# Performance work log

Measured on AMD Instinct MI355X. Metric: run time of the kernel, lower is better.

The kernel has to match this reference:

```python
import jax, jax.numpy as jnp
import numpy as np


def setup_inputs() -> dict:
    key = jax.random.key(0)
    kq, kk, kw, ku, kv = jax.random.split(key, 5)
    B, L, S, H = 32, 2, 4096, 1024
    scale = 1.0 / np.sqrt(H).astype(np.float32)
    return {
        "query": jax.random.normal(kq, (B, L, H), dtype=jnp.float32),
        "keys": jax.random.normal(kk, (B, S, H), dtype=jnp.float32),
        "W": jax.random.normal(kw, (H, H), dtype=jnp.float32) * scale,
        "U": jax.random.normal(ku, (H, H), dtype=jnp.float32) * scale,
        "V": jax.random.normal(kv, (1, H), dtype=jnp.float32) * scale,
    }


def reference(query, keys, W, U, V):
    # query: [B, L, H]; keys: [B, S, H]; torch Linear computes x @ W^T
    q = query[:, -1, :][:, None, :]                      # [B, 1, H]
    wq = jnp.tanh(jnp.einsum('bqh,oh->bqo', q, W))       # [B, 1, H] (tanh only on W q, per source)
    uk = jnp.einsum('bsh,oh->bso', keys, U)              # [B, S, H]
    scores = jnp.einsum('bsh,oh->bso', wq + uk, V)       # [B, S, 1]
    scores = scores[..., 0][:, None, :]                  # [B, 1, S]
    weight = jax.nn.softmax(scores, axis=-1)             # [B, 1, S]
    context = jnp.einsum('bqs,bsh->bqh', weight, keys)   # [B, 1, H]
    return (context, weight)
```

## Files before the change

### kernel.cpp

```cpp
#include <hip/hip_runtime.h>
#include <math.h>

#define HDIM   1024
#define BATCH  32
#define SEQ    4096
#define NB     32
#define SCHUNK (SEQ / NB)
#define NWAVES 4
#define RPW    4
#define PSTR   1028

#define OFF_V 0
#define OFF_P HDIM

__global__ __launch_bounds__(256) void veff_kernel(const float* __restrict__ U,
                                                   const float* __restrict__ V,
                                                   float* __restrict__ ws) {
    const int h  = blockIdx.x * 256 + threadIdx.x;
    const int o0 = blockIdx.y * 64;
    float acc = 0.f;
#pragma unroll 8
    for (int o = o0; o < o0 + 64; ++o) {
        acc += V[o] * U[(long)o * HDIM + h];
    }
    atomicAdd(&ws[OFF_V + h], acc);
}

__global__ __launch_bounds__(256) void score_ctx_kernel(const float* __restrict__ keys,
                                                        float* __restrict__ ws,
                                                        float* __restrict__ out) {
    const int bi    = blockIdx.x;
    const int b     = bi / NB;
    const int chunk = bi % NB;
    const int tid   = threadIdx.x;
    const int w     = tid >> 6;
    const int lane  = tid & 63;

    const float4* v4 = (const float4*)(ws + OFF_V);
    float4 vr[4];
#pragma unroll
    for (int c = 0; c < 4; ++c) vr[c] = v4[c * 64 + lane];

    const float4* k4 = (const float4*)keys;
    const long rowbase = (long)(b * SEQ + chunk * SCHUNK) * (HDIM / 4);

    float4 oacc[4];
#pragma unroll
    for (int c = 0; c < 4; ++c) oacc[c] = make_float4(0.f, 0.f, 0.f, 0.f);
    float l = 0.f;

    float* scores = out + (long)BATCH * HDIM + (long)b * SEQ + chunk * SCHUNK;

    for (int it = 0; it < SCHUNK / (RPW * NWAVES); ++it) {
        const int r0 = it * (RPW * NWAVES) + w * RPW;

        float4 ka[RPW][4];
#pragma unroll
        for (int r = 0; r < RPW; ++r)
#pragma unroll
            for (int c = 0; c < 4; ++c)
                ka[r][c] = k4[rowbase + (long)(r0 + r) * 256 + c * 64 + lane];

        float p[RPW];
#pragma unroll
        for (int r = 0; r < RPW; ++r) {
            float acc = 0.f;
#pragma unroll
            for (int c = 0; c < 4; ++c)
                acc += ka[r][c].x * vr[c].x + ka[r][c].y * vr[c].y
                     + ka[r][c].z * vr[c].z + ka[r][c].w * vr[c].w;
            p[r] = acc;
        }
#pragma unroll
        for (int off = 32; off; off >>= 1) {
#pragma unroll
            for (int r = 0; r < RPW; ++r) p[r] += __shfl_xor(p[r], off, 64);
        }
        if (lane == 0) {
            *(float4*)(scores + r0) = make_float4(p[0], p[1], p[2], p[3]);
        }

        float e[RPW];
#pragma unroll
        for (int r = 0; r < RPW; ++r) e[r] = __expf(p[r]);
        l += e[0] + e[1] + e[2] + e[3];

#pragma unroll
        for (int c = 0; c < 4; ++c) {
            oacc[c].x += e[0]*ka[0][c].x + e[1]*ka[1][c].x + e[2]*ka[2][c].x + e[3]*ka[3][c].x;
            oacc[c].y += e[0]*ka[0][c].y + e[1]*ka[1][c].y + e[2]*ka[2][c].y + e[3]*ka[3][c].y;
            oacc[c].z += e[0]*ka[0][c].z + e[1]*ka[1][c].z + e[2]*ka[2][c].z + e[3]*ka[3][c].z;
            oacc[c].w += e[0]*ka[0][c].w + e[1]*ka[1][c].w + e[2]*ka[2][c].w + e[3]*ka[3][c].w;
        }
    }

    __shared__ float lds_o[NWAVES][HDIM];
    __shared__ float lds_l[NWAVES];

    float4* lo4 = (float4*)lds_o[w];
#pragma unroll
    for (int c = 0; c < 4; ++c) lo4[c * 64 + lane] = oacc[c];
    if (lane == 0) lds_l[w] = l;
    __syncthreads();

    float* part = ws + OFF_P + (long)bi * PSTR;
#pragma unroll
    for (int k = 0; k < HDIM / 256; ++k) {
        const int h = tid + k * 256;
        part[4 + h] = lds_o[0][h] + lds_o[1][h] + lds_o[2][h] + lds_o[3][h];
    }
    if (tid == 0) part[0] = lds_l[0] + lds_l[1] + lds_l[2] + lds_l[3];
}

__global__ __launch_bounds__(256) void combine_kernel(const float* __restrict__ ws,
                                                      float* __restrict__ out) {
    const int b   = blockIdx.x;
    const int tid = threadIdx.x;
    const float* part = ws + OFF_P + (long)b * NB * PSTR;

    float lg = 0.f;
#pragma unroll
    for (int i = 0; i < NB; ++i) lg += part[(long)i * PSTR];
    const float inv_l = 1.f / lg;

#pragma unroll
    for (int k = 0; k < HDIM / 256; ++k) {
        const int h = tid + k * 256;
        float acc = 0.f;
#pragma unroll
        for (int i = 0; i < NB; ++i) acc += part[(long)i * PSTR + 4 + h];
        out[(long)b * HDIM + h] = acc * inv_l;
    }

    float* wout = out + (long)BATCH * HDIM + (long)b * SEQ;
    for (int s = tid; s < SEQ; s += 256) {
        wout[s] = __expf(wout[s]) * inv_l;
    }
}

extern "C" void kernel_launch(void* const* d_in, const int* in_sizes, int n_in,
                              void* d_out, int out_size, void* d_ws, size_t ws_size,
                              hipStream_t stream) {
    const float* keys = (const float*)d_in[1];
    const float* U    = (const float*)d_in[3];
    const float* V    = (const float*)d_in[4];
    float* out = (float*)d_out;
    float* ws  = (float*)d_ws;

    hipMemsetAsync(ws, 0, HDIM * sizeof(float), stream);
    veff_kernel<<<dim3(4, 16), 256, 0, stream>>>(U, V, ws);
    score_ctx_kernel<<<BATCH * NB, 256, 0, stream>>>(keys, ws, out);
    combine_kernel<<<BATCH, 256, 0, stream>>>(ws, out);
}
```

Baseline: 711.3 us.

## Double-buffer key loads, split sequence finer, store exp weights, parallelize combine

```diff
diff --git a/kernel.cpp b/kernel.cpp
--- a/kernel.cpp
+++ b/kernel.cpp
@@ -4,10 +4,11 @@
 #define HDIM   1024
 #define BATCH  32
 #define SEQ    4096
-#define NB     32
+#define NB     64
 #define SCHUNK (SEQ / NB)
 #define NWAVES 4
 #define RPW    4
+#define NIT    (SCHUNK / (RPW * NWAVES))
 #define PSTR   1028
 
 #define OFF_V 0
@@ -49,17 +50,34 @@
     for (int c = 0; c < 4; ++c) oacc[c] = make_float4(0.f, 0.f, 0.f, 0.f);
     float l = 0.f;
 
-    float* scores = out + (long)BATCH * HDIM + (long)b * SEQ + chunk * SCHUNK;
+    float* ew = out + (long)BATCH * HDIM + (long)b * SEQ + chunk * SCHUNK;
 
-    for (int it = 0; it < SCHUNK / (RPW * NWAVES); ++it) {
-        const int r0 = it * (RPW * NWAVES) + w * RPW;
+    float4 ka[2][RPW][4];
 
-        float4 ka[RPW][4];
+    {
+        const int r0 = w * RPW;
 #pragma unroll
         for (int r = 0; r < RPW; ++r)
 #pragma unroll
             for (int c = 0; c < 4; ++c)
-                ka[r][c] = k4[rowbase + (long)(r0 + r) * 256 + c * 64 + lane];
+                ka[0][r][c] = k4[rowbase + (long)(r0 + r) * 256 + c * 64 + lane];
+    }
+
+#pragma unroll
+    for (int it = 0; it < NIT; ++it) {
+        const int cur = it & 1;
+        const int nxt = cur ^ 1;
+
+        if (it + 1 < NIT) {
+            const int r0n = (it + 1) * (RPW * NWAVES) + w * RPW;
+#pragma unroll
+            for (int r = 0; r < RPW; ++r)
+#pragma unroll
+                for (int c = 0; c < 4; ++c)
+                    ka[nxt][r][c] = k4[rowbase + (long)(r0n + r) * 256 + c * 64 + lane];
+        }
+
+        const int r0 = it * (RPW * NWAVES) + w * RPW;
 
         float p[RPW];
 #pragma unroll
@@ -67,8 +85,8 @@
             float acc = 0.f;
 #pragma unroll
             for (int c = 0; c < 4; ++c)
-                acc += ka[r][c].x * vr[c].x + ka[r][c].y * vr[c].y
-                     + ka[r][c].z * vr[c].z + ka[r][c].w * vr[c].w;
+                acc += ka[cur][r][c].x * vr[c].x + ka[cur][r][c].y * vr[c].y
+                     + ka[cur][r][c].z * vr[c].z + ka[cur][r][c].w * vr[c].w;
             p[r] = acc;
         }
 #pragma unroll
@@ -76,21 +94,22 @@
 #pragma unroll
             for (int r = 0; r < RPW; ++r) p[r] += __shfl_xor(p[r], off, 64);
         }
-        if (lane == 0) {
-            *(float4*)(scores + r0) = make_float4(p[0], p[1], p[2], p[3]);
-        }
 
         float e[RPW];
 #pragma unroll
         for (int r = 0; r < RPW; ++r) e[r] = __expf(p[r]);
+
+        if (lane == 0) {
+            *(float4*)(ew + r0) = make_float4(e[0], e[1], e[2], e[3]);
+        }
         l += e[0] + e[1] + e[2] + e[3];
 
 #pragma unroll
         for (int c = 0; c < 4; ++c) {
-            oacc[c].x += e[0]*ka[0][c].x + e[1]*ka[1][c].x + e[2]*ka[2][c].x + e[3]*ka[3][c].x;
-            oacc[c].y += e[0]*ka[0][c].y + e[1]*ka[1][c].y + e[2]*ka[2][c].y + e[3]*ka[3][c].y;
-            oacc[c].z += e[0]*ka[0][c].z + e[1]*ka[1][c].z + e[2]*ka[2][c].z + e[3]*ka[3][c].z;
-            oacc[c].w += e[0]*ka[0][c].w + e[1]*ka[1][c].w + e[2]*ka[2][c].w + e[3]*ka[3][c].w;
+            oacc[c].x += e[0]*ka[cur][0][c].x + e[1]*ka[cur][1][c].x + e[2]*ka[cur][2][c].x + e[3]*ka[cur][3][c].x;
+            oacc[c].y += e[0]*ka[cur][0][c].y + e[1]*ka[cur][1][c].y + e[2]*ka[cur][2][c].y + e[3]*ka[cur][3][c].y;
+            oacc[c].z += e[0]*ka[cur][0][c].z + e[1]*ka[cur][1][c].z + e[2]*ka[cur][2][c].z + e[3]*ka[cur][3][c].z;
+            oacc[c].w += e[0]*ka[cur][0][c].w + e[1]*ka[cur][1][c].w + e[2]*ka[cur][2][c].w + e[3]*ka[cur][3][c].w;
         }
     }
 
@@ -115,6 +134,7 @@
 __global__ __launch_bounds__(256) void combine_kernel(const float* __restrict__ ws,
                                                       float* __restrict__ out) {
     const int b   = blockIdx.x;
+    const int y   = blockIdx.y;
     const int tid = threadIdx.x;
     const float* part = ws + OFF_P + (long)b * NB * PSTR;
 
@@ -123,18 +143,16 @@
     for (int i = 0; i < NB; ++i) lg += part[(long)i * PSTR];
     const float inv_l = 1.f / lg;
 
-#pragma unroll
-    for (int k = 0; k < HDIM / 256; ++k) {
-        const int h = tid + k * 256;
+    if (y < 4) {
+        const int h = y * 256 + tid;
         float acc = 0.f;
 #pragma unroll
         for (int i = 0; i < NB; ++i) acc += part[(long)i * PSTR + 4 + h];
         out[(long)b * HDIM + h] = acc * inv_l;
-    }
-
-    float* wout = out + (long)BATCH * HDIM + (long)b * SEQ;
-    for (int s = tid; s < SEQ; s += 256) {
-        wout[s] = __expf(wout[s]) * inv_l;
+    } else {
+        float* wout = out + (long)BATCH * HDIM + (long)b * SEQ + (y - 4) * 512;
+        wout[tid]       *= inv_l;
+        wout[tid + 256] *= inv_l;
     }
 }
 
@@ -150,5 +168,5 @@
     hipMemsetAsync(ws, 0, HDIM * sizeof(float), stream);
     veff_kernel<<<dim3(4, 16), 256, 0, stream>>>(U, V, ws);
     score_ctx_kernel<<<BATCH * NB, 256, 0, stream>>>(keys, ws, out);
-    combine_kernel<<<BATCH, 256, 0, stream>>>(ws, out);
+    combine_kernel<<<dim3(BATCH, 12), 256, 0, stream>>>(ws, out);
 }
```

After: 712.0 us. About the same (+0.1%).
